# Kernel optimization log

Hardware: AMD Instinct MI355X
Metric: run time of the kernel (lower is better)

## Reference

```python
import jax, jax.numpy as jnp
import numpy as np

NC = 100000   # output rows of the sparse matrix
NT = 100000   # input columns of the sparse matrix
NNZ = 640000  # number of nonzeros (COO entries)
D = 128       # dense feature width


def setup_inputs() -> dict:
    key = jax.random.key(0)
    k1, k2, k3 = jax.random.split(key, 3)
    mat = jax.random.normal(k1, (NT, D), dtype=jnp.float32)
    row = jax.random.randint(k2, (NNZ,), 0, NC, dtype=jnp.int32)
    col = jax.random.randint(k3, (NNZ,), 0, NT, dtype=jnp.int32)
    return {"mat": mat, "row": row, "col": col}


def reference(mat, row, col):
    # Sparse binary (Nc x Nt) @ dense (Nt x D):
    # out[r] += mat[c] for each nonzero (r, c).
    # The TF original batches gather + tensor_scatter_nd_add over the
    # index list; a single gather + segment_sum computes the same result.
    vals = jnp.take(mat, col, axis=0)                      # [nnz, D]
    out = jax.ops.segment_sum(vals, row, num_segments=NC)  # [Nc, D]
    return out
```

## Files before the change

### kernel.cpp

```cpp
#include <hip/hip_runtime.h>


#define NC_CONST 100000
#define NNZ_CONST 640000
#define D_CONST 128
#define OVF_MAX 65536
#define NXCD 8
#define RANGE 12500
#define PLACE_BLOCKS 2048

typedef float v4f __attribute__((ext_vector_type(4)));
typedef unsigned short u16;
typedef u16 v4u16 __attribute__((ext_vector_type(4)));

__device__ __forceinline__ float bf16_to_f32(u16 b) {
    return __uint_as_float((unsigned)b << 16);
}

template <int CAP>
__global__ __launch_bounds__(256) void place_convert_kernel(
    const int* __restrict__ row, const int* __restrict__ col,
    const float* __restrict__ mat,
    int* __restrict__ cnt, int* __restrict__ ovf_cnt,
    int* __restrict__ ovf, int* __restrict__ bucket,
    u16* __restrict__ matb) {
    const int xcd = blockIdx.x % NXCD;
    const int gidx = blockIdx.x / NXCD;
    const int lo = xcd * RANGE;
    const int hi = lo + RANGE;
    const int nthreads = (PLACE_BLOCKS / NXCD) * 256;
    const int4* row4 = reinterpret_cast<const int4*>(row);
    const int4* col4 = reinterpret_cast<const int4*>(col);
    const int n4 = NNZ_CONST / 4;

    for (int i = gidx * 256 + threadIdx.x; i < n4; i += nthreads) {
        int4 r4 = row4[i];
        int4 c4 = col4[i];
        #pragma unroll
        for (int k = 0; k < 4; ++k) {
            int r = (&r4.x)[k];
            if (r >= lo && r < hi) {
                int c = (&c4.x)[k];
                int idx = atomicAdd(&cnt[r], 1);
                if (idx < CAP) {
                    bucket[(size_t)r * CAP + idx] = c;
                } else {
                    int o = atomicAdd(ovf_cnt, 1);
                    if (o < OVF_MAX) { ovf[2 * o] = r; ovf[2 * o + 1] = c; }
                }
            }
        }
    }

    const long long total4 = (long long)NC_CONST * D_CONST / 4;
    const long long stride = (long long)gridDim.x * 256;
    for (long long i = (long long)blockIdx.x * 256 + threadIdx.x;
         i < total4; i += stride) {
        const v4f v = __builtin_nontemporal_load(
            reinterpret_cast<const v4f*>(mat) + i);
        v4u16 o;
        #pragma unroll
        for (int k = 0; k < 4; ++k) {
            unsigned u = __float_as_uint(v[k]);
            o[k] = (u16)((u + 0x7FFFu + ((u >> 16) & 1u)) >> 16);
        }
        reinterpret_cast<v4u16*>(matb)[i] = o;
    }
}

template <int CAP>
__global__ __launch_bounds__(256) void segsum_bf16_kernel(
    const u16* __restrict__ matb, const int* __restrict__ cnt,
    const int* __restrict__ ovf_cnt, const int* __restrict__ ovf,
    const int* __restrict__ bucket, float* __restrict__ out) {
    const int xcd = blockIdx.x % NXCD;
    const int local = blockIdx.x / NXCD;
    int g = xcd * RANGE + local * 8 + (threadIdx.x >> 5);
    int lane = threadIdx.x & 31;
    if (g >= xcd * RANGE + RANGE) return;

    int n = cnt[g];
    if (n > CAP) n = CAP;

    int myc = (lane < n)
        ? __builtin_nontemporal_load(bucket + (size_t)g * CAP + lane) : 0;

    float ax = 0.f, ay = 0.f, az = 0.f, aw = 0.f;
    int j = 0;
    for (; j + 4 <= n; j += 4) {
        int c0 = __shfl(myc, j + 0, 32);
        int c1 = __shfl(myc, j + 1, 32);
        int c2 = __shfl(myc, j + 2, 32);
        int c3 = __shfl(myc, j + 3, 32);
        const v4u16 b0 = reinterpret_cast<const v4u16*>(matb + (size_t)c0 * D_CONST)[lane];
        const v4u16 b1 = reinterpret_cast<const v4u16*>(matb + (size_t)c1 * D_CONST)[lane];
        const v4u16 b2 = reinterpret_cast<const v4u16*>(matb + (size_t)c2 * D_CONST)[lane];
        const v4u16 b3 = reinterpret_cast<const v4u16*>(matb + (size_t)c3 * D_CONST)[lane];
        ax += bf16_to_f32(b0[0]) + bf16_to_f32(b1[0]) + bf16_to_f32(b2[0]) + bf16_to_f32(b3[0]);
        ay += bf16_to_f32(b0[1]) + bf16_to_f32(b1[1]) + bf16_to_f32(b2[1]) + bf16_to_f32(b3[1]);
        az += bf16_to_f32(b0[2]) + bf16_to_f32(b1[2]) + bf16_to_f32(b2[2]) + bf16_to_f32(b3[2]);
        aw += bf16_to_f32(b0[3]) + bf16_to_f32(b1[3]) + bf16_to_f32(b2[3]) + bf16_to_f32(b3[3]);
    }
    for (; j < n; ++j) {
        int c = __shfl(myc, j, 32);
        const v4u16 b = reinterpret_cast<const v4u16*>(matb + (size_t)c * D_CONST)[lane];
        ax += bf16_to_f32(b[0]);
        ay += bf16_to_f32(b[1]);
        az += bf16_to_f32(b[2]);
        aw += bf16_to_f32(b[3]);
    }

    int novf = *ovf_cnt;
    if (novf > 0) {
        if (novf > OVF_MAX) novf = OVF_MAX;
        for (int o = 0; o < novf; ++o) {
            if (ovf[2 * o] == g) {
                int c = ovf[2 * o + 1];
                const v4u16 b = reinterpret_cast<const v4u16*>(matb + (size_t)c * D_CONST)[lane];
                ax += bf16_to_f32(b[0]);
                ay += bf16_to_f32(b[1]);
                az += bf16_to_f32(b[2]);
                aw += bf16_to_f32(b[3]);
            }
        }
    }

    v4f r;
    r.x = ax; r.y = ay; r.z = az; r.w = aw;
    __builtin_nontemporal_store(
        r, reinterpret_cast<v4f*>(out + (size_t)g * D_CONST) + lane);
}

template <int CAP>
__global__ __launch_bounds__(256) void segsum_xcd_kernel(
    const float* __restrict__ mat, const int* __restrict__ cnt,
    const int* __restrict__ ovf_cnt, const int* __restrict__ ovf,
    const int* __restrict__ bucket, float* __restrict__ out) {
    const int xcd = blockIdx.x % NXCD;
    const int local = blockIdx.x / NXCD;
    int g = xcd * RANGE + local * 8 + (threadIdx.x >> 5);
    int lane = threadIdx.x & 31;
    if (g >= xcd * RANGE + RANGE) return;

    int n = cnt[g];
    if (n > CAP) n = CAP;
    int myc = (lane < n) ? bucket[(size_t)g * CAP + lane] : 0;

    float ax = 0.f, ay = 0.f, az = 0.f, aw = 0.f;
    for (int j = 0; j < n; ++j) {
        int c = __shfl(myc, j, 32);
        const float4 v =
            reinterpret_cast<const float4*>(mat + (size_t)c * D_CONST)[lane];
        ax += v.x; ay += v.y; az += v.z; aw += v.w;
    }
    int novf = *ovf_cnt;
    if (novf > OVF_MAX) novf = OVF_MAX;
    for (int o = 0; o < novf; ++o) {
        if (ovf[2 * o] == g) {
            int c = ovf[2 * o + 1];
            const float4 v =
                reinterpret_cast<const float4*>(mat + (size_t)c * D_CONST)[lane];
            ax += v.x; ay += v.y; az += v.z; aw += v.w;
        }
    }
    v4f r;
    r.x = ax; r.y = ay; r.z = az; r.w = aw;
    __builtin_nontemporal_store(
        r, reinterpret_cast<v4f*>(out + (size_t)g * D_CONST) + lane);
}

template <int CAP>
__global__ __launch_bounds__(256) void place_xcd_kernel(
    const int* __restrict__ row, const int* __restrict__ col,
    int* __restrict__ cnt, int* __restrict__ ovf_cnt,
    int* __restrict__ ovf, int* __restrict__ bucket) {
    const int xcd = blockIdx.x % NXCD;
    const int gidx = blockIdx.x / NXCD;
    const int lo = xcd * RANGE;
    const int hi = lo + RANGE;
    const int nthreads = (PLACE_BLOCKS / NXCD) * 256;
    const int4* row4 = reinterpret_cast<const int4*>(row);
    const int4* col4 = reinterpret_cast<const int4*>(col);
    const int n4 = NNZ_CONST / 4;

    for (int i = gidx * 256 + threadIdx.x; i < n4; i += nthreads) {
        int4 r4 = row4[i];
        int4 c4 = col4[i];
        #pragma unroll
        for (int k = 0; k < 4; ++k) {
            int r = (&r4.x)[k];
            if (r >= lo && r < hi) {
                int c = (&c4.x)[k];
                int idx = atomicAdd(&cnt[r], 1);
                if (idx < CAP) {
                    bucket[(size_t)r * CAP + idx] = c;
                } else {
                    int o = atomicAdd(ovf_cnt, 1);
                    if (o < OVF_MAX) { ovf[2 * o] = r; ovf[2 * o + 1] = c; }
                }
            }
        }
    }
}

__global__ __launch_bounds__(256) void scatter_add_kernel(
    const float* __restrict__ mat, const int* __restrict__ row,
    const int* __restrict__ col, float* __restrict__ out) {
    int gid = blockIdx.x * blockDim.x + threadIdx.x;
    int nz = gid >> 5;
    int lane = gid & 31;
    if (nz >= NNZ_CONST) return;
    int r = row[nz];
    int c = col[nz];
    const float4 v =
        reinterpret_cast<const float4*>(mat + (size_t)c * D_CONST)[lane];
    float* o = out + (size_t)r * D_CONST + (size_t)lane * 4;
    atomicAdd(o + 0, v.x);
    atomicAdd(o + 1, v.y);
    atomicAdd(o + 2, v.z);
    atomicAdd(o + 3, v.w);
}

extern "C" void kernel_launch(void* const* d_in, const int* in_sizes, int n_in,
                              void* d_out, int out_size, void* d_ws, size_t ws_size,
                              hipStream_t stream) {
    const float* mat = (const float*)d_in[0];
    const int* row   = (const int*)d_in[1];
    const int* col   = (const int*)d_in[2];
    float* out = (float*)d_out;

    constexpr int CAP = 32;
    const size_t ints_common =
        (size_t)NC_CONST + 1 + 2 * OVF_MAX + (size_t)NC_CONST * CAP;
    const size_t need_bf16 =
        (size_t)NC_CONST * D_CONST * sizeof(u16) + ints_common * sizeof(int);
    const size_t need_fp32 = ints_common * sizeof(int);

    const int seg_blocks = ((RANGE + 7) / 8) * NXCD;

    if (ws_size >= need_bf16) {
        u16* matb    = (u16*)d_ws;
        int* cnt     = (int*)(matb + (size_t)NC_CONST * D_CONST);
        int* ovf_cnt = cnt + NC_CONST;
        int* ovf     = ovf_cnt + 1;
        int* bucket  = ovf + 2 * OVF_MAX;

        (void)hipMemsetAsync(cnt, 0, (size_t)(NC_CONST + 1) * sizeof(int), stream);

        place_convert_kernel<CAP><<<PLACE_BLOCKS, 256, 0, stream>>>(
            row, col, mat, cnt, ovf_cnt, ovf, bucket, matb);

        segsum_bf16_kernel<CAP><<<seg_blocks, 256, 0, stream>>>(
            matb, cnt, ovf_cnt, ovf, bucket, out);
    } else if (ws_size >= need_fp32) {
        int* cnt     = (int*)d_ws;
        int* ovf_cnt = cnt + NC_CONST;
        int* ovf     = ovf_cnt + 1;
        int* bucket  = ovf + 2 * OVF_MAX;

        (void)hipMemsetAsync(cnt, 0, (size_t)(NC_CONST + 1) * sizeof(int), stream);

        place_xcd_kernel<CAP><<<PLACE_BLOCKS, 256, 0, stream>>>(
            row, col, cnt, ovf_cnt, ovf, bucket);
        segsum_xcd_kernel<CAP><<<seg_blocks, 256, 0, stream>>>(
            mat, cnt, ovf_cnt, ovf, bucket, out);
    } else {
        (void)hipMemsetAsync(out, 0, (size_t)out_size * sizeof(float), stream);
        const long long total = (long long)NNZ_CONST * 32;
        scatter_add_kernel<<<(int)((total + 255) / 256), 256, 0, stream>>>(
            mat, row, col, out);
    }
}
```

Baseline: 162.8 us.

## Split placement and bf16 conversion blocks, pad counters, skip col loads

The fused place/convert kernel now gives 512 blocks to the fp32-to-bf16 conversion of the dense matrix and the remaining 1536 blocks to COO bucket placement, instead of every block doing both phases in sequence. Placement threads skip loading the col vector when none of their four rows fall in the block's XCD range. Per-row counters are padded to a stride of 8 ints so atomics on nearby rows no longer share a cache line. The padding makes the counter array and its memset eight times larger, and fewer blocks now do placement.

```diff
diff --git a/kernel.cpp b/kernel.cpp
--- a/kernel.cpp
+++ b/kernel.cpp
@@ -7,7 +7,10 @@
 #define OVF_MAX 65536
 #define NXCD 8
 #define RANGE 12500
-#define PLACE_BLOCKS 2048
+#define TOTAL_BLOCKS 2048
+#define CONV_BLOCKS 512
+#define PLACE_BLOCKS (TOTAL_BLOCKS - CONV_BLOCKS)
+#define CNT_STRIDE 8
 
 typedef float v4f __attribute__((ext_vector_type(4)));
 typedef unsigned short u16;
@@ -24,6 +27,25 @@
     int* __restrict__ cnt, int* __restrict__ ovf_cnt,
     int* __restrict__ ovf, int* __restrict__ bucket,
     u16* __restrict__ matb) {
+    if (blockIdx.x >= PLACE_BLOCKS) {
+        const int cb = blockIdx.x - PLACE_BLOCKS;
+        const long long total4 = (long long)NC_CONST * D_CONST / 4;
+        const long long stride = (long long)CONV_BLOCKS * 256;
+        for (long long i = (long long)cb * 256 + threadIdx.x;
+             i < total4; i += stride) {
+            const v4f v = __builtin_nontemporal_load(
+                reinterpret_cast<const v4f*>(mat) + i);
+            v4u16 o;
+            #pragma unroll
+            for (int k = 0; k < 4; ++k) {
+                unsigned u = __float_as_uint(v[k]);
+                o[k] = (u16)((u + 0x7FFFu + ((u >> 16) & 1u)) >> 16);
+            }
+            reinterpret_cast<v4u16*>(matb)[i] = o;
+        }
+        return;
+    }
+
     const int xcd = blockIdx.x % NXCD;
     const int gidx = blockIdx.x / NXCD;
     const int lo = xcd * RANGE;
@@ -35,13 +57,18 @@
 
     for (int i = gidx * 256 + threadIdx.x; i < n4; i += nthreads) {
         int4 r4 = row4[i];
+        bool in0 = (r4.x >= lo && r4.x < hi);
+        bool in1 = (r4.y >= lo && r4.y < hi);
+        bool in2 = (r4.z >= lo && r4.z < hi);
+        bool in3 = (r4.w >= lo && r4.w < hi);
+        if (!(in0 | in1 | in2 | in3)) continue;
         int4 c4 = col4[i];
         #pragma unroll
         for (int k = 0; k < 4; ++k) {
             int r = (&r4.x)[k];
             if (r >= lo && r < hi) {
                 int c = (&c4.x)[k];
-                int idx = atomicAdd(&cnt[r], 1);
+                int idx = atomicAdd(&cnt[(size_t)r * CNT_STRIDE], 1);
                 if (idx < CAP) {
                     bucket[(size_t)r * CAP + idx] = c;
                 } else {
@@ -51,21 +78,6 @@
             }
         }
     }
-
-    const long long total4 = (long long)NC_CONST * D_CONST / 4;
-    const long long stride = (long long)gridDim.x * 256;
-    for (long long i = (long long)blockIdx.x * 256 + threadIdx.x;
-         i < total4; i += stride) {
-        const v4f v = __builtin_nontemporal_load(
-            reinterpret_cast<const v4f*>(mat) + i);
-        v4u16 o;
-        #pragma unroll
-        for (int k = 0; k < 4; ++k) {
-            unsigned u = __float_as_uint(v[k]);
-            o[k] = (u16)((u + 0x7FFFu + ((u >> 16) & 1u)) >> 16);
-        }
-        reinterpret_cast<v4u16*>(matb)[i] = o;
-    }
 }
 
 template <int CAP>
@@ -79,7 +91,7 @@
     int lane = threadIdx.x & 31;
     if (g >= xcd * RANGE + RANGE) return;
 
-    int n = cnt[g];
+    int n = cnt[(size_t)g * CNT_STRIDE];
     if (n > CAP) n = CAP;
 
     int myc = (lane < n)
@@ -178,7 +190,7 @@
     const int gidx = blockIdx.x / NXCD;
     const int lo = xcd * RANGE;
     const int hi = lo + RANGE;
-    const int nthreads = (PLACE_BLOCKS / NXCD) * 256;
+    const int nthreads = (2048 / NXCD) * 256;
     const int4* row4 = reinterpret_cast<const int4*>(row);
     const int4* col4 = reinterpret_cast<const int4*>(col);
     const int n4 = NNZ_CONST / 4;
@@ -230,24 +242,25 @@
     float* out = (float*)d_out;
 
     constexpr int CAP = 32;
-    const size_t ints_common =
-        (size_t)NC_CONST + 1 + 2 * OVF_MAX + (size_t)NC_CONST * CAP;
+    const size_t cnt_pad_ints = (size_t)NC_CONST * CNT_STRIDE;
     const size_t need_bf16 =
-        (size_t)NC_CONST * D_CONST * sizeof(u16) + ints_common * sizeof(int);
-    const size_t need_fp32 = ints_common * sizeof(int);
+        (size_t)NC_CONST * D_CONST * sizeof(u16) +
+        (cnt_pad_ints + 1 + 2 * OVF_MAX + (size_t)NC_CONST * CAP) * sizeof(int);
+    const size_t need_fp32 =
+        ((size_t)NC_CONST + 1 + 2 * OVF_MAX + (size_t)NC_CONST * CAP) * sizeof(int);
 
     const int seg_blocks = ((RANGE + 7) / 8) * NXCD;
 
     if (ws_size >= need_bf16) {
         u16* matb    = (u16*)d_ws;
         int* cnt     = (int*)(matb + (size_t)NC_CONST * D_CONST);
-        int* ovf_cnt = cnt + NC_CONST;
+        int* ovf_cnt = cnt + cnt_pad_ints;
         int* ovf     = ovf_cnt + 1;
         int* bucket  = ovf + 2 * OVF_MAX;
 
-        (void)hipMemsetAsync(cnt, 0, (size_t)(NC_CONST + 1) * sizeof(int), stream);
-
-        place_convert_kernel<CAP><<<PLACE_BLOCKS, 256, 0, stream>>>(
+        (void)hipMemsetAsync(cnt, 0, (cnt_pad_ints + 1) * sizeof(int), stream);
+
+        place_convert_kernel<CAP><<<TOTAL_BLOCKS, 256, 0, stream>>>(
             row, col, mat, cnt, ovf_cnt, ovf, bucket, matb);
 
         segsum_bf16_kernel<CAP><<<seg_blocks, 256, 0, stream>>>(
@@ -259,8 +272,7 @@
         int* bucket  = ovf + 2 * OVF_MAX;
 
         (void)hipMemsetAsync(cnt, 0, (size_t)(NC_CONST + 1) * sizeof(int), stream);
-
-        place_xcd_kernel<CAP><<<PLACE_BLOCKS, 256, 0, stream>>>(
+        place_xcd_kernel<CAP><<<2048, 256, 0, stream>>>(
             row, col, cnt, ovf_cnt, ovf, bucket);
         segsum_xcd_kernel<CAP><<<seg_blocks, 256, 0, stream>>>(
             mat, cnt, ovf_cnt, ovf, bucket, out);
```

Result: slower. 167.0 us (+2.5%).
